# Performance work log

Measured on AMD Instinct MI355X. Metric: run time of the kernel, lower is better.

Reference implementation:

```python
import jax, jax.numpy as jnp
import numpy as np

B, N, G = 32, 1024, 8   # batch, Nvecs (= k_in), Nglobals
K_OUT, H = 128, 128     # MLP output width, hidden width
D_IN = 1 + N + G        # MLP input width: [u, norm, dots]


def setup_inputs() -> dict:
    key = jax.random.key(0)
    ks = jax.random.split(key, 8)
    x = jax.random.uniform(ks[0], (B, N, 3), dtype=jnp.float32)  # positive coords -> dots >= 0
    u = jax.random.normal(ks[1], (B, G), dtype=jnp.float32)
    s0 = 1.0 / np.sqrt(D_IN)
    s1 = 1.0 / np.sqrt(H)
    W0 = jax.random.normal(ks[2], (D_IN, H), dtype=jnp.float32) * s0
    b0 = jnp.zeros((H,), dtype=jnp.float32)
    W1 = jax.random.normal(ks[3], (H, H), dtype=jnp.float32) * s1
    b1 = jnp.zeros((H,), dtype=jnp.float32)
    W2 = jax.random.normal(ks[4], (H, K_OUT), dtype=jnp.float32) * s1
    b2 = jnp.zeros((K_OUT,), dtype=jnp.float32)
    return {"x": x, "u": u, "W0": W0, "b0": b0, "W1": W1, "b1": b1, "W2": W2, "b2": b2}


def reference(x, u, W0, b0, W1, b1, W2, b2):
    # x: [B, N, 3], u: [B, G]
    norms = jnp.linalg.norm(x, axis=-1, keepdims=True)            # [B, N, 1]
    dots = jnp.sqrt(jnp.einsum('bid,bjd->bij', x, x))             # [B, N, N]
    u_rep = jnp.broadcast_to(u[:, None, :], (x.shape[0], x.shape[1], u.shape[-1]))
    scalars = jnp.concatenate([u_rep, norms, dots], axis=-1)      # [B, N, G+1+N]
    # MLP (Linear -> LeakyReLU -> Linear -> LeakyReLU -> Linear)
    h = jax.nn.leaky_relu(scalars @ W0 + b0)
    h = jax.nn.leaky_relu(h @ W1 + b1)
    fk = h @ W2 + b2                                              # [B, N, K_OUT]
    # outer product 'bio,bid->biod' followed by mean over i == fused contraction
    out = jnp.einsum('bio,bid->bod', fk, x) / x.shape[1]          # [B, K_OUT, 3]
    return out
```

## Files before the change

kernel.cpp:

```cpp
#include <hip/hip_runtime.h>
#include <hip/hip_fp16.h>

typedef _Float16 f16;
typedef f16 f16x4 __attribute__((ext_vector_type(4)));
typedef f16 f16x8 __attribute__((ext_vector_type(8)));
typedef float f32x4 __attribute__((ext_vector_type(4)));

#define NN 1024

#define IMG2_OFF  0
#define W8_OFF    327680
#define BIAS0_OFF 328192

__global__ __launch_bounds__(256) void prep_kernel(
    const float* __restrict__ u,  const float* __restrict__ W0,
    const float* __restrict__ b0, const float* __restrict__ W1,
    const float* __restrict__ W2,
    f16* __restrict__ img2, float* __restrict__ w8v, float* __restrict__ bias0,
    float* __restrict__ outp)
{
    const int t = threadIdx.x;
    const int blk = blockIdx.x;
    if (blk < 160) {
        int flat = blk * 1024 + t * 4;
        int c   = flat >> 13;
        int rem = flat & 8191;
        int s0  = rem & 7;
        int lm  = (rem >> 3) & 15;
        int q   = (rem >> 7) & 3;
        int ks  = (rem >> 9) & 1;
        int nt  = (rem >> 10) & 3;
        int wn  = (rem >> 12) & 1;
        int n = wn * 64 + nt * 16 + lm;
        f16x4 v;
#pragma unroll
        for (int e = 0; e < 4; ++e) {
            int k = ks * 32 + q * 8 + s0 + e;
            float val;
            if (c < 16)       val = W0[(9 + c * 64 + k) * 128 + n];
            else if (c < 18)  val = W1[((c - 16) * 64 + k) * 128 + n];
            else              val = W2[((c - 18) * 64 + k) * 128 + n];
            v[e] = (f16)val;
        }
        *(f16x4*)&img2[flat] = v;
    } else if (blk < 176) {
        int idx = (blk - 160) * 256 + t;
        int b = idx >> 7, h = idx & 127;
        float s = b0[h];
#pragma unroll
        for (int g = 0; g < 8; ++g) s += u[b * 8 + g] * W0[g * 128 + h];
        bias0[idx] = s;
    } else if (blk == 176) {
        if (t < 128) w8v[t] = W0[8 * 128 + t];
    } else {
        int idx = (blk - 177) * 1024 + t * 4;
        if (idx < 12288) { float4 z = {0.f, 0.f, 0.f, 0.f}; *(float4*)&outp[idx] = z; }
    }
}

__global__ __launch_bounds__(256, 4) void fused_kernel(
    const float* __restrict__ x, const float* __restrict__ b1p,
    const float* __restrict__ b2p, const f16* __restrict__ img2,
    const float* __restrict__ w8v, const float* __restrict__ bias0,
    float* __restrict__ outp)
{
    __shared__ __align__(16) f16 Dsh[2][32 * 64];
    __shared__ __align__(16) f16 xjsh[1024 * 4];
    __shared__ __align__(16) float xi[32 * 4];
    __shared__ float normv[32];
    __shared__ float biass[128];
    __shared__ float w8s[128];

    const int t = threadIdx.x;
    const int b = blockIdx.x >> 5;
    const int i0 = (blockIdx.x & 31) * 32;

    {
        const float* xb = x + (size_t)b * NN * 3;
        float4 v0 = *(const float4*)(xb + t * 12);
        float4 v1 = *(const float4*)(xb + t * 12 + 4);
        float4 v2 = *(const float4*)(xb + t * 12 + 8);
        f16x4 r0; r0[0] = (f16)v0.x; r0[1] = (f16)v0.y; r0[2] = (f16)v0.z; r0[3] = (f16)0;
        f16x4 r1; r1[0] = (f16)v0.w; r1[1] = (f16)v1.x; r1[2] = (f16)v1.y; r1[3] = (f16)0;
        f16x4 r2; r2[0] = (f16)v1.z; r2[1] = (f16)v1.w; r2[2] = (f16)v2.x; r2[3] = (f16)0;
        f16x4 r3; r3[0] = (f16)v2.y; r3[1] = (f16)v2.z; r3[2] = (f16)v2.w; r3[3] = (f16)0;
        *(f16x4*)&xjsh[(t * 4 + 0) * 4] = r0;
        *(f16x4*)&xjsh[(t * 4 + 1) * 4] = r1;
        *(f16x4*)&xjsh[(t * 4 + 2) * 4] = r2;
        *(f16x4*)&xjsh[(t * 4 + 3) * 4] = r3;
    }
    if (t < 96) {
        int i = t / 3, d = t - i * 3;
        xi[i * 4 + d] = x[(size_t)(b * NN + i0 + i) * 3 + d];
    }
    if (t >= 128 && t < 256) { biass[t - 128] = bias0[b * 128 + (t - 128)]; }
    if (t >= 96 && t < 224 && t - 96 < 128) { w8s[t - 96] = w8v[t - 96]; }
    __syncthreads();
    if (t < 32) {
        float a0 = xi[t * 4], a1 = xi[t * 4 + 1], a2 = xi[t * 4 + 2];
        normv[t] = __builtin_amdgcn_sqrtf(a0 * a0 + a1 * a1 + a2 * a2);
    }

    const int lane = t & 63, wv = t >> 6;
    const int wm = wv >> 1, wn = wv & 1;
    const int lm = lane & 15, q = lane >> 4;

    f16x4 bi[2];
#pragma unroll
    for (int it = 0; it < 2; ++it) {
        f16x4 v; v[0] = (f16)0; v[1] = (f16)0; v[2] = (f16)0; v[3] = (f16)0;
        if (q == 0) {
            int ii = it * 16 + lm;
            v[0] = (f16)xi[ii * 4];
            v[1] = (f16)xi[ii * 4 + 1];
            v[2] = (f16)xi[ii * 4 + 2];
        }
        bi[it] = v;
    }

    f32x4 acc[4];
    auto zero_acc = [&]() {
#pragma unroll
        for (int nt = 0; nt < 4; ++nt)
#pragma unroll
            for (int e = 0; e < 4; ++e) acc[nt][e] = 0.f;
    };
    zero_acc();

    auto dotstore = [&](int jc, int buf) {
        f16x4 ajv; ajv[0] = (f16)0; ajv[1] = (f16)0; ajv[2] = (f16)0; ajv[3] = (f16)0;
        if (q == 0)
            ajv = *(const f16x4*)&xjsh[(jc * 64 + wv * 16 + lm) * 4];
#pragma unroll
        for (int it = 0; it < 2; ++it) {
            f32x4 z; z[0] = 0.f; z[1] = 0.f; z[2] = 0.f; z[3] = 0.f;
            f32x4 cg = __builtin_amdgcn_mfma_f32_16x16x16f16(ajv, bi[it], z, 0, 0, 0);
            f16x4 dv;
#pragma unroll
            for (int r = 0; r < 4; ++r)
                dv[r] = (f16)__builtin_amdgcn_sqrtf(fmaxf(cg[r], 0.f));
            int row = it * 16 + lm;
            int colstart = wv * 16 + q * 4;
            int addr = row * 64 + (((colstart & ~7) ^ ((row & 7) << 3)) | (colstart & 7));
            *(f16x4*)&Dsh[buf][addr] = dv;
        }
    };

    auto kstep = [&](int dbuf, int c, int dotjc, int dotbuf) {
        const f16* wb = img2 + (size_t)(c * 2 + wn) * 4096 + lane * 8;
        f16x8 bf[4][2];
#pragma unroll
        for (int nt = 0; nt < 4; ++nt)
#pragma unroll
            for (int ks = 0; ks < 2; ++ks)
                bf[nt][ks] = *(const f16x8*)(wb + (nt * 2 + ks) * 512);
        f16x8 af[2];
#pragma unroll
        for (int ks = 0; ks < 2; ++ks) {
            int row = wm * 16 + lm;
            int col = ks * 32 + q * 8;
            af[ks] = *(const f16x8*)(Dsh[dbuf] + row * 64 + (col ^ ((row & 7) << 3)));
        }
        if (dotjc >= 0) dotstore(dotjc, dotbuf);
#pragma unroll
        for (int ks = 0; ks < 2; ++ks)
#pragma unroll
            for (int nt = 0; nt < 4; ++nt)
                acc[nt] = __builtin_amdgcn_mfma_f32_16x16x32_f16(
                    af[ks], bf[nt][ks], acc[nt], 0, 0, 0);
    };

    dotstore(0, 0);
    __syncthreads();

#pragma unroll 2
    for (int jc = 0; jc < 16; ++jc) {
        kstep(jc & 1, jc, (jc < 15) ? jc + 1 : -1, (jc & 1) ^ 1);
        __syncthreads();
    }

#pragma unroll
    for (int nt = 0; nt < 4; ++nt) {
        const int h = wn * 64 + nt * 16 + lm;
        const float bh = biass[h], w8h = w8s[h];
        const int hh = h & 63;
#pragma unroll
        for (int r = 0; r < 4; ++r) {
            int i = wm * 16 + q * 4 + r;
            float val = acc[nt][r] + bh + normv[i] * w8h;
            val = val > 0.f ? val : 0.01f * val;
            int addr = i * 64 + (((hh & ~7) ^ ((i & 7) << 3)) | (hh & 7));
            Dsh[wn][addr] = (f16)val;
        }
    }
    __syncthreads();

    zero_acc();
#pragma unroll
    for (int hb = 0; hb < 2; ++hb)
        kstep(hb, 16 + hb, -1, 0);
    __syncthreads();

#pragma unroll
    for (int nt = 0; nt < 4; ++nt) {
        const int h = wn * 64 + nt * 16 + lm;
        const float bh = b1p[h];
        const int hh = h & 63;
#pragma unroll
        for (int r = 0; r < 4; ++r) {
            int i = wm * 16 + q * 4 + r;
            float val = acc[nt][r] + bh;
            val = val > 0.f ? val : 0.01f * val;
            int addr = i * 64 + (((hh & ~7) ^ ((i & 7) << 3)) | (hh & 7));
            Dsh[wn][addr] = (f16)val;
        }
    }
    __syncthreads();

    zero_acc();
#pragma unroll
    for (int hb = 0; hb < 2; ++hb)
        kstep(hb, 18 + hb, -1, 0);

    float p[4][3];
#pragma unroll
    for (int nt = 0; nt < 4; ++nt)
#pragma unroll
        for (int d = 0; d < 3; ++d) p[nt][d] = 0.f;
    float bo[4];
#pragma unroll
    for (int nt = 0; nt < 4; ++nt) bo[nt] = b2p[wn * 64 + nt * 16 + lm];
#pragma unroll
    for (int r = 0; r < 4; ++r) {
        int i = wm * 16 + q * 4 + r;
        float x0 = xi[i * 4], x1 = xi[i * 4 + 1], x2 = xi[i * 4 + 2];
#pragma unroll
        for (int nt = 0; nt < 4; ++nt) {
            float fkv = acc[nt][r] + bo[nt];
            p[nt][0] = fmaf(fkv, x0, p[nt][0]);
            p[nt][1] = fmaf(fkv, x1, p[nt][1]);
            p[nt][2] = fmaf(fkv, x2, p[nt][2]);
        }
    }
#pragma unroll
    for (int nt = 0; nt < 4; ++nt)
#pragma unroll
        for (int d = 0; d < 3; ++d) {
            float s = p[nt][d];
            s += __shfl_xor(s, 16);
            s += __shfl_xor(s, 32);
            if (q == 0) {
                int o = wn * 64 + nt * 16 + lm;
                atomicAdd(&outp[(b * 128 + o) * 3 + d], s * (1.0f / 1024.0f));
            }
        }
}

extern "C" void kernel_launch(void* const* d_in, const int* in_sizes, int n_in,
                              void* d_out, int out_size, void* d_ws, size_t ws_size,
                              hipStream_t stream) {
    const float* x  = (const float*)d_in[0];
    const float* u  = (const float*)d_in[1];
    const float* W0 = (const float*)d_in[2];
    const float* b0 = (const float*)d_in[3];
    const float* W1 = (const float*)d_in[4];
    const float* b1 = (const float*)d_in[5];
    const float* W2 = (const float*)d_in[6];
    const float* b2 = (const float*)d_in[7];

    char* ws = (char*)d_ws;
    f16*   img2  = (f16*)(ws + IMG2_OFF);
    float* w8v   = (float*)(ws + W8_OFF);
    float* bias0 = (float*)(ws + BIAS0_OFF);
    float* out   = (float*)d_out;

    prep_kernel<<<189, 256, 0, stream>>>(u, W0, b0, W1, W2, img2, w8v, bias0, out);
    fused_kernel<<<1024, 256, 0, stream>>>(x, b1, b2, img2, w8v, bias0, out);
}
```

Before: 104.7 us.

## Materialize full dots tile in LDS to remove per-chunk barriers

Replaces the double-buffered per-64-column pipeline, which interleaved dot computation with the first GEMM and synced every chunk, with two phases. All 32x1024 sqrt-dot values are first computed into a 64KB swizzled LDS tile, then the first-layer GEMM runs over all 16 chunks without intermediate barriers. Hidden activations move to a separate padded LDS buffer. LDS per block grows to about 75KB and launch bounds drop to 2 blocks per CU, which lowers occupancy and loses the overlap of dot computation with MFMA work.

Result: slower. 125.2 us (+19.6%).

```diff
diff --git a/kernel.cpp b/kernel.cpp
--- a/kernel.cpp
+++ b/kernel.cpp
@@ -58,14 +58,14 @@
     }
 }
 
-__global__ __launch_bounds__(256, 4) void fused_kernel(
+__global__ __launch_bounds__(256, 2) void fused_kernel(
     const float* __restrict__ x, const float* __restrict__ b1p,
     const float* __restrict__ b2p, const f16* __restrict__ img2,
     const float* __restrict__ w8v, const float* __restrict__ bias0,
     float* __restrict__ outp)
 {
-    __shared__ __align__(16) f16 Dsh[2][32 * 64];
-    __shared__ __align__(16) f16 xjsh[1024 * 4];
+    __shared__ __align__(16) f16 Dsh[32 * 1024];
+    __shared__ __align__(16) f16 Hx[32 * 136];
     __shared__ __align__(16) float xi[32 * 4];
     __shared__ float normv[32];
     __shared__ float biass[128];
@@ -84,17 +84,16 @@
         f16x4 r1; r1[0] = (f16)v0.w; r1[1] = (f16)v1.x; r1[2] = (f16)v1.y; r1[3] = (f16)0;
         f16x4 r2; r2[0] = (f16)v1.z; r2[1] = (f16)v1.w; r2[2] = (f16)v2.x; r2[3] = (f16)0;
         f16x4 r3; r3[0] = (f16)v2.y; r3[1] = (f16)v2.z; r3[2] = (f16)v2.w; r3[3] = (f16)0;
-        *(f16x4*)&xjsh[(t * 4 + 0) * 4] = r0;
-        *(f16x4*)&xjsh[(t * 4 + 1) * 4] = r1;
-        *(f16x4*)&xjsh[(t * 4 + 2) * 4] = r2;
-        *(f16x4*)&xjsh[(t * 4 + 3) * 4] = r3;
+        *(f16x4*)&Hx[(t * 4 + 0) * 4] = r0;
+        *(f16x4*)&Hx[(t * 4 + 1) * 4] = r1;
+        *(f16x4*)&Hx[(t * 4 + 2) * 4] = r2;
+        *(f16x4*)&Hx[(t * 4 + 3) * 4] = r3;
     }
     if (t < 96) {
         int i = t / 3, d = t - i * 3;
         xi[i * 4 + d] = x[(size_t)(b * NN + i0 + i) * 3 + d];
     }
-    if (t >= 128 && t < 256) { biass[t - 128] = bias0[b * 128 + (t - 128)]; }
-    if (t >= 96 && t < 224 && t - 96 < 128) { w8s[t - 96] = w8v[t - 96]; }
+    if (t >= 128) { biass[t - 128] = bias0[b * 128 + (t - 128)]; w8s[t - 128] = w8v[t - 128]; }
     __syncthreads();
     if (t < 32) {
         float a0 = xi[t * 4], a1 = xi[t * 4 + 1], a2 = xi[t * 4 + 2];
@@ -127,10 +126,11 @@
     };
     zero_acc();
 
-    auto dotstore = [&](int jc, int buf) {
+#pragma unroll 4
+    for (int jc = 0; jc < 16; ++jc) {
         f16x4 ajv; ajv[0] = (f16)0; ajv[1] = (f16)0; ajv[2] = (f16)0; ajv[3] = (f16)0;
         if (q == 0)
-            ajv = *(const f16x4*)&xjsh[(jc * 64 + wv * 16 + lm) * 4];
+            ajv = *(const f16x4*)&Hx[(jc * 64 + wv * 16 + lm) * 4];
 #pragma unroll
         for (int it = 0; it < 2; ++it) {
             f32x4 z; z[0] = 0.f; z[1] = 0.f; z[2] = 0.f; z[3] = 0.f;
@@ -140,13 +140,15 @@
             for (int r = 0; r < 4; ++r)
                 dv[r] = (f16)__builtin_amdgcn_sqrtf(fmaxf(cg[r], 0.f));
             int row = it * 16 + lm;
-            int colstart = wv * 16 + q * 4;
-            int addr = row * 64 + (((colstart & ~7) ^ ((row & 7) << 3)) | (colstart & 7));
-            *(f16x4*)&Dsh[buf][addr] = dv;
-        }
-    };
-
-    auto kstep = [&](int dbuf, int c, int dotjc, int dotbuf) {
+            int col = jc * 64 + wv * 16 + q * 4;
+            int addr = row * 1024 + (((col & ~7) ^ ((row & 7) << 3)) | (col & 7));
+            *(f16x4*)&Dsh[addr] = dv;
+        }
+    }
+    __syncthreads();
+
+#pragma unroll 4
+    for (int c = 0; c < 16; ++c) {
         const f16* wb = img2 + (size_t)(c * 2 + wn) * 4096 + lane * 8;
         f16x8 bf[4][2];
 #pragma unroll
@@ -155,72 +157,100 @@
             for (int ks = 0; ks < 2; ++ks)
                 bf[nt][ks] = *(const f16x8*)(wb + (nt * 2 + ks) * 512);
         f16x8 af[2];
-#pragma unroll
-        for (int ks = 0; ks < 2; ++ks) {
+        {
             int row = wm * 16 + lm;
-            int col = ks * 32 + q * 8;
-            af[ks] = *(const f16x8*)(Dsh[dbuf] + row * 64 + (col ^ ((row & 7) << 3)));
-        }
-        if (dotjc >= 0) dotstore(dotjc, dotbuf);
+#pragma unroll
+            for (int ks = 0; ks < 2; ++ks) {
+                int col = c * 64 + ks * 32 + q * 8;
+                af[ks] = *(const f16x8*)(Dsh + row * 1024 + (col ^ ((row & 7) << 3)));
+            }
+        }
 #pragma unroll
         for (int ks = 0; ks < 2; ++ks)
 #pragma unroll
             for (int nt = 0; nt < 4; ++nt)
                 acc[nt] = __builtin_amdgcn_mfma_f32_16x16x32_f16(
                     af[ks], bf[nt][ks], acc[nt], 0, 0, 0);
-    };
-
-    dotstore(0, 0);
-    __syncthreads();
-
-#pragma unroll 2
-    for (int jc = 0; jc < 16; ++jc) {
-        kstep(jc & 1, jc, (jc < 15) ? jc + 1 : -1, (jc & 1) ^ 1);
-        __syncthreads();
     }
 
 #pragma unroll
     for (int nt = 0; nt < 4; ++nt) {
         const int h = wn * 64 + nt * 16 + lm;
         const float bh = biass[h], w8h = w8s[h];
-        const int hh = h & 63;
 #pragma unroll
         for (int r = 0; r < 4; ++r) {
             int i = wm * 16 + q * 4 + r;
             float val = acc[nt][r] + bh + normv[i] * w8h;
             val = val > 0.f ? val : 0.01f * val;
-            int addr = i * 64 + (((hh & ~7) ^ ((i & 7) << 3)) | (hh & 7));
-            Dsh[wn][addr] = (f16)val;
+            Hx[i * 136 + h] = (f16)val;
         }
     }
     __syncthreads();
 
     zero_acc();
 #pragma unroll
-    for (int hb = 0; hb < 2; ++hb)
-        kstep(hb, 16 + hb, -1, 0);
+    for (int hb = 0; hb < 2; ++hb) {
+        const f16* wb = img2 + (size_t)((16 + hb) * 2 + wn) * 4096 + lane * 8;
+        f16x8 bf[4][2];
+#pragma unroll
+        for (int nt = 0; nt < 4; ++nt)
+#pragma unroll
+            for (int ks = 0; ks < 2; ++ks)
+                bf[nt][ks] = *(const f16x8*)(wb + (nt * 2 + ks) * 512);
+        f16x8 af[2];
+        {
+            int row = wm * 16 + lm;
+#pragma unroll
+            for (int ks = 0; ks < 2; ++ks)
+                af[ks] = *(const f16x8*)(Hx + row * 136 + hb * 64 + ks * 32 + q * 8);
+        }
+#pragma unroll
+        for (int ks = 0; ks < 2; ++ks)
+#pragma unroll
+            for (int nt = 0; nt < 4; ++nt)
+                acc[nt] = __builtin_amdgcn_mfma_f32_16x16x32_f16(
+                    af[ks], bf[nt][ks], acc[nt], 0, 0, 0);
+    }
     __syncthreads();
 
 #pragma unroll
     for (int nt = 0; nt < 4; ++nt) {
         const int h = wn * 64 + nt * 16 + lm;
         const float bh = b1p[h];
-        const int hh = h & 63;
 #pragma unroll
         for (int r = 0; r < 4; ++r) {
             int i = wm * 16 + q * 4 + r;
             float val = acc[nt][r] + bh;
             val = val > 0.f ? val : 0.01f * val;
-            int addr = i * 64 + (((hh & ~7) ^ ((i & 7) << 3)) | (hh & 7));
-            Dsh[wn][addr] = (f16)val;
+            Hx[i * 136 + h] = (f16)val;
         }
     }
     __syncthreads();
 
     zero_acc();
 #pragma unroll
-    for (int hb = 0; hb < 2; ++hb)
-        kstep(hb, 18 + hb, -1, 0);
+    for (int hb = 0; hb < 2; ++hb) {
+        const f16* wb = img2 + (size_t)((18 + hb) * 2 + wn) * 4096 + lane * 8;
+        f16x8 bf[4][2];
+#pragma unroll
+        for (int nt = 0; nt < 4; ++nt)
+#pragma unroll
+            for (int ks = 0; ks < 2; ++ks)
+                bf[nt][ks] = *(const f16x8*)(wb + (nt * 2 + ks) * 512);
+        f16x8 af[2];
+        {
+            int row = wm * 16 + lm;
+#pragma unroll
+            for (int ks = 0; ks < 2; ++ks)
+                af[ks] = *(const f16x8*)(Hx + row * 136 + hb * 64 + ks * 32 + q * 8);
+        }
+#pragma unroll
+        for (int ks = 0; ks < 2; ++ks)
+#pragma unroll
+            for (int nt = 0; nt < 4; ++nt)
+                acc[nt] = __builtin_amdgcn_mfma_f32_16x16x32_f16(
+                    af[ks], bf[nt][ks], acc[nt], 0, 0, 0);
+    }
 
     float p[4][3];
 #pragma unroll
```
